# Optimization experiments

Hardware: AMD Instinct MI355X
Metric: run time of the kernel (lower is better)

Reference implementation:

```python
import jax, jax.numpy as jnp
import numpy as np

SEQ, D_IN, D_OUT = 8192, 1024, 1024


def setup_inputs() -> dict:
    key = jax.random.key(0)
    kx, kq, kk, kv = jax.random.split(key, 4)
    # torch nn.Linear weights have shape (out_features, in_features)
    s = 1.0 / np.sqrt(D_IN)
    return {
        "x": jax.random.normal(kx, (SEQ, D_IN), dtype=jnp.float32),
        "Wq": jax.random.uniform(kq, (D_OUT, D_IN), dtype=jnp.float32, minval=-s, maxval=s),
        "Wk": jax.random.uniform(kk, (D_OUT, D_IN), dtype=jnp.float32, minval=-s, maxval=s),
        "Wv": jax.random.uniform(kv, (D_OUT, D_IN), dtype=jnp.float32, minval=-s, maxval=s),
    }


def reference(x, Wq, Wk, Wv):
    # Linear (no bias): y = x @ W.T
    q = x @ Wq.T          # [S, D_OUT]
    k = x @ Wk.T          # [S, D_OUT]
    v = x @ Wv.T          # [S, D_OUT]
    scale = 1.0 / jnp.sqrt(jnp.asarray(k.shape[-1], dtype=x.dtype))
    scores = (q @ k.T) * scale            # [S, S]
    weights = jax.nn.softmax(scores, axis=-1)
    return weights @ v                    # [S, D_OUT]
```

## Files before the change

### kernel.cpp

```cpp
#include <hip/hip_runtime.h>
#include <hip/hip_bf16.h>
#include <stdint.h>


#define SEQ 8192
#define DMODEL 1024
#define LOG2E 1.44269504088896340736f
#define GROUP_M 8

typedef __bf16 bf16_t;
typedef __bf16 bf16x8 __attribute__((ext_vector_type(8)));
typedef float f32x4 __attribute__((ext_vector_type(4)));

__global__ __launch_bounds__(256)
void convert_f32_bf16(const float* __restrict__ in, bf16_t* __restrict__ out, long n) {
    long i = ((long)blockIdx.x * 256 + threadIdx.x) * 4;
    if (i + 3 < n) {
        const float4 v = *(const float4*)(in + i);
        union { ushort4 u; bf16_t b[4]; } p;
        p.b[0] = (bf16_t)v.x; p.b[1] = (bf16_t)v.y;
        p.b[2] = (bf16_t)v.z; p.b[3] = (bf16_t)v.w;
        *(ushort4*)(out + i) = p.u;
    }
}

__global__ __launch_bounds__(256)
void add_f32(float* __restrict__ out, const float* __restrict__ part, long n) {
    long i = ((long)blockIdx.x * 256 + threadIdx.x) * 4;
    if (i + 3 < n) {
        float4 a = *(const float4*)(out + i);
        const float4 b = *(const float4*)(part + i);
        a.x += b.x; a.y += b.y; a.z += b.z; a.w += b.w;
        *(float4*)(out + i) = a;
    }
}

__global__ __launch_bounds__(256)
void zero_f32(float* __restrict__ p, int n) {
    int i = blockIdx.x * 256 + threadIdx.x;
    if (i < n) p[i] = 0.0f;
}

template <typename OutT, int MODE>
__global__ __launch_bounds__(256, 3)
void gemm_nt(const bf16_t* __restrict__ A, const bf16_t* __restrict__ B,
             OutT* __restrict__ C0, OutT* __restrict__ C1,
             float* __restrict__ lsum,
             int M, int N, int Kps, int lda, int ldb, int ldc,
             long plane, int cshift, float alpha)
{
    __shared__ bf16_t As[128 * 64];
    __shared__ bf16_t Bs[128 * 64];

    const int tid  = threadIdx.x;
    const int wave = tid >> 6;
    const int lane = tid & 63;

    const int nbm = M >> 7, nbn = N >> 7;
    const int tiles = nbm * nbn;
    int bid = blockIdx.x;
    const int sid = bid / tiles;
    bid -= sid * tiles;
    const long kbase = (long)sid * Kps;
    OutT* __restrict__ C = sid ? C1 : C0;

    const int per_group = GROUP_M * nbn;
    const int gid   = bid / per_group;
    const int rem   = bid - gid * per_group;
    const int first = gid * GROUP_M;
    const int gsz   = min(nbm - first, GROUP_M);
    const int bm    = first + rem % gsz;
    const int bn    = rem / gsz;
    const long row0 = (long)bm * 128;
    const long col0 = (long)bn * 128;

    const int wm = (wave >> 1) * 64;
    const int wn = (wave & 1) * 64;
    const int lr = lane & 15;
    const int lq = lane >> 4;

    f32x4 acc[4][4] = {};

    for (int k0 = 0; k0 < Kps; k0 += 64) {
        #pragma unroll
        for (int i = 0; i < 4; ++i) {
            const int c = i * 256 + wave * 64 + lane;
            const int r = c >> 3, p = c & 7;
            const int l = (p + r) & 7;
            const bf16_t* ga = A + (row0 + r) * (long)lda + kbase + k0 + l * 8;
            const bf16_t* gb = B + (col0 + r) * (long)ldb + kbase + k0 + l * 8;
            __builtin_amdgcn_global_load_lds(
                (const __attribute__((address_space(1))) uint32_t*)ga,
                (__attribute__((address_space(3))) uint32_t*)(As + (long)c * 8),
                16, 0, 0);
            __builtin_amdgcn_global_load_lds(
                (const __attribute__((address_space(1))) uint32_t*)gb,
                (__attribute__((address_space(3))) uint32_t*)(Bs + (long)c * 8),
                16, 0, 0);
        }
        __syncthreads();

        #pragma unroll
        for (int t = 0; t < 2; ++t) {
            bf16x8 af[4], bfr[4];
            #pragma unroll
            for (int mi = 0; mi < 4; ++mi) {
                const int r = wm + mi * 16 + lr;
                const int p = (t * 4 + lq - r) & 7;
                af[mi] = *(const bf16x8*)(As + (long)r * 64 + p * 8);
            }
            #pragma unroll
            for (int ni = 0; ni < 4; ++ni) {
                const int r = wn + ni * 16 + lr;
                const int p = (t * 4 + lq - r) & 7;
                bfr[ni] = *(const bf16x8*)(Bs + (long)r * 64 + p * 8);
            }
            #pragma unroll
            for (int mi = 0; mi < 4; ++mi)
                #pragma unroll
                for (int ni = 0; ni < 4; ++ni)
                    acc[mi][ni] = __builtin_amdgcn_mfma_f32_16x16x32_bf16(
                        af[mi], bfr[ni], acc[mi][ni], 0, 0, 0);
        }
        __syncthreads();
    }

    OutT* __restrict__ Cb = C + (col0 >> cshift) * plane;
    const int ccol0 = (int)(col0 & (((long)1 << cshift) - 1));

    if (MODE == 1) {
        #pragma unroll
        for (int mi = 0; mi < 4; ++mi)
            #pragma unroll
            for (int rg = 0; rg < 4; ++rg) {
                const long r = row0 + wm + mi * 16 + lq * 4 + rg;
                float part = 0.f;
                #pragma unroll
                for (int ni = 0; ni < 4; ++ni) {
                    const int c = ccol0 + wn + ni * 16 + lr;
                    const float e = exp2f(alpha * acc[mi][ni][rg]);
                    part += e;
                    Cb[r * (long)ldc + c] = (OutT)e;
                }
                part += __shfl_xor(part, 1);
                part += __shfl_xor(part, 2);
                part += __shfl_xor(part, 4);
                part += __shfl_xor(part, 8);
                if (lr == 0) atomicAdd(&lsum[r], part);
            }
    } else if (MODE == 2) {
        #pragma unroll
        for (int mi = 0; mi < 4; ++mi)
            #pragma unroll
            for (int rg = 0; rg < 4; ++rg) {
                const long r = row0 + wm + mi * 16 + lq * 4 + rg;
                const float inv = 1.0f / lsum[r];
                #pragma unroll
                for (int ni = 0; ni < 4; ++ni) {
                    const int c = ccol0 + wn + ni * 16 + lr;
                    Cb[r * (long)ldc + c] = (OutT)(acc[mi][ni][rg] * inv);
                }
            }
    } else {
        #pragma unroll
        for (int mi = 0; mi < 4; ++mi)
            #pragma unroll
            for (int ni = 0; ni < 4; ++ni)
                #pragma unroll
                for (int rg = 0; rg < 4; ++rg) {
                    const long r = row0 + wm + mi * 16 + lq * 4 + rg;
                    const int  c = ccol0 + wn + ni * 16 + lr;
                    Cb[r * (long)ldc + c] = (OutT)(alpha * acc[mi][ni][rg]);
                }
    }
}

__global__ __launch_bounds__(256)
void transpose_bf16(const bf16_t* __restrict__ in, bf16_t* __restrict__ out,
                    int R, int ldin, int ldout)
{
    __shared__ bf16_t tile[32][33];
    const int tx = threadIdx.x & 31;
    const int ty = threadIdx.x >> 5;
    const int c0 = blockIdx.x * 32;
    const int r0 = blockIdx.y * 32;
    #pragma unroll
    for (int j = 0; j < 32; j += 8)
        tile[ty + j][tx] = in[(long)(r0 + ty + j) * ldin + c0 + tx];
    __syncthreads();
    #pragma unroll
    for (int j = 0; j < 32; j += 8)
        out[(long)(c0 + ty + j) * ldout + r0 + tx] = tile[tx][ty + j];
}

extern "C" void kernel_launch(void* const* d_in, const int* in_sizes, int n_in,
                              void* d_out, int out_size, void* d_ws, size_t ws_size,
                              hipStream_t stream)
{
    const float* x  = (const float*)d_in[0];
    const float* Wq = (const float*)d_in[1];
    const float* Wk = (const float*)d_in[2];
    const float* Wv = (const float*)d_in[3];
    float* out = (float*)d_out;

    char* ws = (char*)d_ws;
    const long XN = (long)SEQ * DMODEL;
    const long WN = (long)DMODEL * DMODEL;
    const long SN = (long)SEQ * SEQ;

    bf16_t* xb   = (bf16_t*)ws;
    bf16_t* wcat = (bf16_t*)(ws + XN * 2);
    bf16_t* qb   = (bf16_t*)(ws + XN * 2 + WN * 6);
    bf16_t* kb   = qb + XN;
    bf16_t* vb   = qb + 2 * XN;
    bf16_t* Sb   = (bf16_t*)(ws + XN * 2 + WN * 6 + XN * 6);
    float*  pvp  = (float*)(ws + XN * 2 + WN * 6 + XN * 6 + SN * 2);
    float*  lsum = (float*)(ws + XN * 2 + WN * 6 + XN * 6 + SN * 2 + XN * 4);
    bf16_t* vtb  = xb;

    const size_t base_need = (size_t)(XN * 2 + WN * 6 + XN * 6 + SN * 2);
    const bool use_split = ws_size >= base_need + XN * 4 + SEQ * 4;
    if (!use_split) lsum = (float*)(ws + base_need);

    convert_f32_bf16<<<(int)(XN / 4 / 256), 256, 0, stream>>>(x,  xb, XN);
    convert_f32_bf16<<<(int)(WN / 4 / 256), 256, 0, stream>>>(Wq, wcat,          WN);
    convert_f32_bf16<<<(int)(WN / 4 / 256), 256, 0, stream>>>(Wk, wcat + WN,     WN);
    convert_f32_bf16<<<(int)(WN / 4 / 256), 256, 0, stream>>>(Wv, wcat + 2 * WN, WN);
    zero_f32<<<SEQ / 256, 256, 0, stream>>>(lsum, SEQ);

    dim3 blk(256);
    gemm_nt<bf16_t, 0><<<(SEQ / 128) * (3 * DMODEL / 128), blk, 0, stream>>>(
        xb, wcat, qb, qb, nullptr, SEQ, 3 * DMODEL, DMODEL,
        DMODEL, DMODEL, DMODEL, XN, 10, 1.0f);

    transpose_bf16<<<dim3(DMODEL / 32, SEQ / 32), blk, 0, stream>>>(
        vb, vtb, SEQ, DMODEL, SEQ);

    gemm_nt<bf16_t, 1><<<(SEQ / 128) * (SEQ / 128), blk, 0, stream>>>(
        qb, kb, Sb, Sb, lsum, SEQ, SEQ, DMODEL,
        DMODEL, DMODEL, SEQ, 0, 30, 0.03125f * LOG2E);

    if (use_split) {
        gemm_nt<float, 2><<<2 * (SEQ / 128) * (DMODEL / 128), blk, 0, stream>>>(
            Sb, vtb, out, pvp, lsum, SEQ, DMODEL, SEQ / 2,
            SEQ, SEQ, DMODEL, 0, 30, 1.0f);
        add_f32<<<(int)(XN / 4 / 256), 256, 0, stream>>>(out, pvp, XN);
    } else {
        gemm_nt<float, 2><<<(SEQ / 128) * (DMODEL / 128), blk, 0, stream>>>(
            Sb, vtb, out, out, lsum, SEQ, DMODEL, SEQ,
            SEQ, SEQ, DMODEL, 0, 30, 1.0f);
    }
}
```

Measured before the change: 495.8 us.

## Enlarge GEMM tiles to 256x256 with double-buffered LDS prefetch pipeline

Switches the shared NT GEMM from 128x128 tiles with 256 threads to 256x256 tiles with 512 threads, each wave computing a 128x64 sub-tile. It adds a two-stage LDS double buffer so the global-to-LDS loads for step k+2 are issued between MFMA groups, and uses explicit vmcnt/lgkmcnt waits plus s_setprio. The aim is to hide global load latency and cut the number of times each operand is reloaded. The cost is 128KB of LDS per block, which limits occupancy to one block per CU. Grids also shrink, so the PV and QKV GEMMs launch only about 256 and 384 blocks.

```diff
diff --git a/kernel.cpp b/kernel.cpp
--- a/kernel.cpp
+++ b/kernel.cpp
@@ -42,21 +42,21 @@
 }
 
 template <typename OutT, int MODE>
-__global__ __launch_bounds__(256, 3)
+__global__ __launch_bounds__(512, 2)
 void gemm_nt(const bf16_t* __restrict__ A, const bf16_t* __restrict__ B,
              OutT* __restrict__ C0, OutT* __restrict__ C1,
              float* __restrict__ lsum,
              int M, int N, int Kps, int lda, int ldb, int ldc,
              long plane, int cshift, float alpha)
 {
-    __shared__ bf16_t As[128 * 64];
-    __shared__ bf16_t Bs[128 * 64];
+    __shared__ bf16_t As[2][256 * 64];
+    __shared__ bf16_t Bs[2][256 * 64];
 
     const int tid  = threadIdx.x;
     const int wave = tid >> 6;
     const int lane = tid & 63;
 
-    const int nbm = M >> 7, nbn = N >> 7;
+    const int nbm = M >> 8, nbn = N >> 8;
     const int tiles = nbm * nbn;
     int bid = blockIdx.x;
     const int sid = bid / tiles;
@@ -71,66 +71,129 @@
     const int gsz   = min(nbm - first, GROUP_M);
     const int bm    = first + rem % gsz;
     const int bn    = rem / gsz;
-    const long row0 = (long)bm * 128;
-    const long col0 = (long)bn * 128;
-
-    const int wm = (wave >> 1) * 64;
-    const int wn = (wave & 1) * 64;
+    const long row0 = (long)bm * 256;
+    const long col0 = (long)bn * 256;
+
+    const int wm = (wave >> 2) * 128;
+    const int wn = (wave & 3) * 64;
     const int lr = lane & 15;
     const int lq = lane >> 4;
 
-    f32x4 acc[4][4] = {};
-
-    for (int k0 = 0; k0 < Kps; k0 += 64) {
-        #pragma unroll
-        for (int i = 0; i < 4; ++i) {
-            const int c = i * 256 + wave * 64 + lane;
-            const int r = c >> 3, p = c & 7;
-            const int l = (p + r) & 7;
-            const bf16_t* ga = A + (row0 + r) * (long)lda + kbase + k0 + l * 8;
-            const bf16_t* gb = B + (col0 + r) * (long)ldb + kbase + k0 + l * 8;
-            __builtin_amdgcn_global_load_lds(
-                (const __attribute__((address_space(1))) uint32_t*)ga,
-                (__attribute__((address_space(3))) uint32_t*)(As + (long)c * 8),
-                16, 0, 0);
-            __builtin_amdgcn_global_load_lds(
-                (const __attribute__((address_space(1))) uint32_t*)gb,
-                (__attribute__((address_space(3))) uint32_t*)(Bs + (long)c * 8),
-                16, 0, 0);
-        }
-        __syncthreads();
-
-        #pragma unroll
-        for (int t = 0; t < 2; ++t) {
-            bf16x8 af[4], bfr[4];
-            #pragma unroll
-            for (int mi = 0; mi < 4; ++mi) {
-                const int r = wm + mi * 16 + lr;
-                const int p = (t * 4 + lq - r) & 7;
-                af[mi] = *(const bf16x8*)(As + (long)r * 64 + p * 8);
-            }
-            #pragma unroll
-            for (int ni = 0; ni < 4; ++ni) {
-                const int r = wn + ni * 16 + lr;
-                const int p = (t * 4 + lq - r) & 7;
-                bfr[ni] = *(const bf16x8*)(Bs + (long)r * 64 + p * 8);
-            }
-            #pragma unroll
-            for (int mi = 0; mi < 4; ++mi)
-                #pragma unroll
-                for (int ni = 0; ni < 4; ++ni)
-                    acc[mi][ni] = __builtin_amdgcn_mfma_f32_16x16x32_bf16(
-                        af[mi], bfr[ni], acc[mi][ni], 0, 0, 0);
-        }
-        __syncthreads();
-    }
+    const int rt = tid >> 3;
+    const int sl = ((tid & 7) + rt) & 7;
+    const bf16_t* pa = A + (row0 + rt) * (long)lda + kbase + sl * 8;
+    const bf16_t* pb = B + (col0 + rt) * (long)ldb + kbase + sl * 8;
+
+    const int p0  = (lq - lr) & 7;
+    const int p1  = p0 ^ 4;
+    const int oA0 = (wm + lr) * 64 + p0 * 8;
+    const int oA1 = (wm + lr) * 64 + p1 * 8;
+    const int oB0 = (wn + lr) * 64 + p0 * 8;
+    const int oB1 = (wn + lr) * 64 + p1 * 8;
+
+    const int nt = Kps >> 6;
+
+    f32x4 acc[8][4] = {};
+
+#define STAGE2(kt, bsel, i0)                                                    \
+    {                                                                           \
+        _Pragma("unroll")                                                       \
+        for (int ii = 0; ii < 2; ++ii) {                                        \
+            const int i = (i0) + ii;                                            \
+            const bf16_t* ga = pa + (long)(kt) * 64 + (long)i * 64 * lda;       \
+            const bf16_t* gb = pb + (long)(kt) * 64 + (long)i * 64 * ldb;       \
+            __builtin_amdgcn_global_load_lds(                                   \
+                (const __attribute__((address_space(1))) uint32_t*)ga,          \
+                (__attribute__((address_space(3))) uint32_t*)(As[bsel] + i * 4096 + tid * 8), \
+                16, 0, 0);                                                      \
+            __builtin_amdgcn_global_load_lds(                                   \
+                (const __attribute__((address_space(1))) uint32_t*)gb,          \
+                (__attribute__((address_space(3))) uint32_t*)(Bs[bsel] + i * 4096 + tid * 8), \
+                16, 0, 0);                                                      \
+        }                                                                       \
+    }
+
+    STAGE2(0, 0, 0); STAGE2(0, 0, 2);
+    if (nt > 1) { STAGE2(1, 1, 0); STAGE2(1, 1, 2); }
+
+    int cur = 0;
+    for (int t = 0; t < nt; ++t) {
+        const bf16_t* as = As[cur];
+        const bf16_t* bs = Bs[cur];
+
+        if (t + 1 < nt) { asm volatile("s_waitcnt vmcnt(8)" ::: "memory"); }
+        else            { asm volatile("s_waitcnt vmcnt(0)" ::: "memory"); }
+        __builtin_amdgcn_s_barrier();
+
+        bf16x8 a0[8], b0[4], a1[8], b1[4];
+        #pragma unroll
+        for (int mi = 0; mi < 8; ++mi)
+            a0[mi] = *(const bf16x8*)(as + oA0 + mi * 1024);
+        #pragma unroll
+        for (int ni = 0; ni < 4; ++ni)
+            b0[ni] = *(const bf16x8*)(bs + oB0 + ni * 1024);
+
+        __builtin_amdgcn_s_setprio(1);
+        #pragma unroll
+        for (int mi = 0; mi < 4; ++mi)
+            #pragma unroll
+            for (int ni = 0; ni < 4; ++ni)
+                acc[mi][ni] = __builtin_amdgcn_mfma_f32_16x16x32_bf16(
+                    a0[mi], b0[ni], acc[mi][ni], 0, 0, 0);
+        __builtin_amdgcn_s_setprio(0);
+
+        #pragma unroll
+        for (int mi = 0; mi < 8; ++mi)
+            a1[mi] = *(const bf16x8*)(as + oA1 + mi * 1024);
+        #pragma unroll
+        for (int ni = 0; ni < 4; ++ni)
+            b1[ni] = *(const bf16x8*)(bs + oB1 + ni * 1024);
+
+        __builtin_amdgcn_s_setprio(1);
+        #pragma unroll
+        for (int mi = 4; mi < 8; ++mi)
+            #pragma unroll
+            for (int ni = 0; ni < 4; ++ni)
+                acc[mi][ni] = __builtin_amdgcn_mfma_f32_16x16x32_bf16(
+                    a0[mi], b0[ni], acc[mi][ni], 0, 0, 0);
+        __builtin_amdgcn_s_setprio(0);
+
+        asm volatile("s_waitcnt lgkmcnt(0)" ::: "memory");
+        __builtin_amdgcn_sched_barrier(0);
+        __builtin_amdgcn_s_barrier();
+
+        if (t + 2 < nt) STAGE2(t + 2, cur, 0);
+
+        __builtin_amdgcn_s_setprio(1);
+        #pragma unroll
+        for (int mi = 0; mi < 4; ++mi)
+            #pragma unroll
+            for (int ni = 0; ni < 4; ++ni)
+                acc[mi][ni] = __builtin_amdgcn_mfma_f32_16x16x32_bf16(
+                    a1[mi], b1[ni], acc[mi][ni], 0, 0, 0);
+        __builtin_amdgcn_s_setprio(0);
+
+        if (t + 2 < nt) STAGE2(t + 2, cur, 2);
+
+        __builtin_amdgcn_s_setprio(1);
+        #pragma unroll
+        for (int mi = 4; mi < 8; ++mi)
+            #pragma unroll
+            for (int ni = 0; ni < 4; ++ni)
+                acc[mi][ni] = __builtin_amdgcn_mfma_f32_16x16x32_bf16(
+                    a1[mi], b1[ni], acc[mi][ni], 0, 0, 0);
+        __builtin_amdgcn_s_setprio(0);
+
+        cur ^= 1;
+    }
+#undef STAGE2
 
     OutT* __restrict__ Cb = C + (col0 >> cshift) * plane;
     const int ccol0 = (int)(col0 & (((long)1 << cshift) - 1));
 
     if (MODE == 1) {
         #pragma unroll
-        for (int mi = 0; mi < 4; ++mi)
+        for (int mi = 0; mi < 8; ++mi)
             #pragma unroll
             for (int rg = 0; rg < 4; ++rg) {
                 const long r = row0 + wm + mi * 16 + lq * 4 + rg;
@@ -150,7 +213,7 @@
             }
     } else if (MODE == 2) {
         #pragma unroll
-        for (int mi = 0; mi < 4; ++mi)
+        for (int mi = 0; mi < 8; ++mi)
             #pragma unroll
             for (int rg = 0; rg < 4; ++rg) {
                 const long r = row0 + wm + mi * 16 + lq * 4 + rg;
@@ -163,7 +226,7 @@
             }
     } else {
         #pragma unroll
-        for (int mi = 0; mi < 4; ++mi)
+        for (int mi = 0; mi < 8; ++mi)
             #pragma unroll
             for (int ni = 0; ni < 4; ++ni)
                 #pragma unroll
@@ -228,25 +291,26 @@
     convert_f32_bf16<<<(int)(WN / 4 / 256), 256, 0, stream>>>(Wv, wcat + 2 * WN, WN);
     zero_f32<<<SEQ / 256, 256, 0, stream>>>(lsum, SEQ);
 
-    dim3 blk(256);
-    gemm_nt<bf16_t, 0><<<(SEQ / 128) * (3 * DMODEL / 128), blk, 0, stream>>>(
+    dim3 blk256(256);
+    dim3 blk512(512);
+    gemm_nt<bf16_t, 0><<<(SEQ / 256) * (3 * DMODEL / 256), blk512, 0, stream>>>(
         xb, wcat, qb, qb, nullptr, SEQ, 3 * DMODEL, DMODEL,
         DMODEL, DMODEL, DMODEL, XN, 10, 1.0f);
 
-    transpose_bf16<<<dim3(DMODEL / 32, SEQ / 32), blk, 0, stream>>>(
+    transpose_bf16<<<dim3(DMODEL / 32, SEQ / 32), blk256, 0, stream>>>(
         vb, vtb, SEQ, DMODEL, SEQ);
 
-    gemm_nt<bf16_t, 1><<<(SEQ / 128) * (SEQ / 128), blk, 0, stream>>>(
+    gemm_nt<bf16_t, 1><<<(SEQ / 256) * (SEQ / 256), blk512, 0, stream>>>(
         qb, kb, Sb, Sb, lsum, SEQ, SEQ, DMODEL,
         DMODEL, DMODEL, SEQ, 0, 30, 0.03125f * LOG2E);
 
     if (use_split) {
-        gemm_nt<float, 2><<<2 * (SEQ / 128) * (DMODEL / 128), blk, 0, stream>>>(
+        gemm_nt<float, 2><<<2 * (SEQ / 256) * (DMODEL / 256), blk512, 0, stream>>>(
             Sb, vtb, out, pvp, lsum, SEQ, DMODEL, SEQ / 2,
             SEQ, SEQ, DMODEL, 0, 30, 1.0f);
         add_f32<<<(int)(XN / 4 / 256), 256, 0, stream>>>(out, pvp, XN);
     } else {
-        gemm_nt<float, 2><<<(SEQ / 128) * (DMODEL / 128), blk, 0, stream>>>(
+        gemm_nt<float, 2><<<(SEQ / 256) * (DMODEL / 256), blk512, 0, stream>>>(
             Sb, vtb, out, out, lsum, SEQ, DMODEL, SEQ,
             SEQ, SEQ, DMODEL, 0, 30, 1.0f);
     }
```

After: 474.9 us. 1.04x faster.

## Halve GEMM K-tile to 32, precompute swizzled addresses, remap blocks across XCDs

Applied to the files above, without the earlier changes.

Shrinks the K step of the bf16 GEMM from 64 to 32. That halves LDS per block and lets the load and fragment addresses be computed once with a new 4-way swizzle. It also remaps block IDs so consecutive tiles are spread across 8 chiplets (XCDs) for better L2 locality. The smaller K tile means twice as many barrier pairs per unit of work, with less MFMA work between them to hide load latency. It may raise occupancy, but sync overhead could dominate.

```diff
diff --git a/kernel.cpp b/kernel.cpp
--- a/kernel.cpp
+++ b/kernel.cpp
@@ -49,8 +49,8 @@
              int M, int N, int Kps, int lda, int ldb, int ldc,
              long plane, int cshift, float alpha)
 {
-    __shared__ bf16_t As[128 * 64];
-    __shared__ bf16_t Bs[128 * 64];
+    __shared__ bf16_t As[128 * 32];
+    __shared__ bf16_t Bs[128 * 32];
 
     const int tid  = threadIdx.x;
     const int wave = tid >> 6;
@@ -63,6 +63,9 @@
     bid -= sid * tiles;
     const long kbase = (long)sid * Kps;
     OutT* __restrict__ C = sid ? C1 : C0;
+
+    const int cpx = tiles >> 3;
+    bid = (bid & 7) * cpx + (bid >> 3);
 
     const int per_group = GROUP_M * nbn;
     const int gid   = bid / per_group;
@@ -79,49 +82,46 @@
     const int lr = lane & 15;
     const int lq = lane >> 4;
 
+    const int rt = tid >> 2;
+    const int sl = ((tid & 3) + ((tid >> 4) & 3)) & 3;
+    const bf16_t* pa = A + (row0 + rt) * (long)lda + kbase + sl * 8;
+    const bf16_t* pb = B + (col0 + rt) * (long)ldb + kbase + sl * 8;
+
+    const int p0  = (lq - ((lr >> 2) & 3)) & 3;
+    const int oA  = (wm + lr) * 32 + p0 * 8;
+    const int oB  = (wn + lr) * 32 + p0 * 8;
+
     f32x4 acc[4][4] = {};
 
-    for (int k0 = 0; k0 < Kps; k0 += 64) {
-        #pragma unroll
-        for (int i = 0; i < 4; ++i) {
-            const int c = i * 256 + wave * 64 + lane;
-            const int r = c >> 3, p = c & 7;
-            const int l = (p + r) & 7;
-            const bf16_t* ga = A + (row0 + r) * (long)lda + kbase + k0 + l * 8;
-            const bf16_t* gb = B + (col0 + r) * (long)ldb + kbase + k0 + l * 8;
+    for (int k0 = 0; k0 < Kps; k0 += 32) {
+        #pragma unroll
+        for (int i = 0; i < 2; ++i) {
+            const bf16_t* ga = pa + k0 + (long)i * 64 * lda;
+            const bf16_t* gb = pb + k0 + (long)i * 64 * ldb;
             __builtin_amdgcn_global_load_lds(
                 (const __attribute__((address_space(1))) uint32_t*)ga,
-                (__attribute__((address_space(3))) uint32_t*)(As + (long)c * 8),
+                (__attribute__((address_space(3))) uint32_t*)(As + (long)(i * 256 + tid) * 8),
                 16, 0, 0);
             __builtin_amdgcn_global_load_lds(
                 (const __attribute__((address_space(1))) uint32_t*)gb,
-                (__attribute__((address_space(3))) uint32_t*)(Bs + (long)c * 8),
+                (__attribute__((address_space(3))) uint32_t*)(Bs + (long)(i * 256 + tid) * 8),
                 16, 0, 0);
         }
         __syncthreads();
 
-        #pragma unroll
-        for (int t = 0; t < 2; ++t) {
-            bf16x8 af[4], bfr[4];
-            #pragma unroll
-            for (int mi = 0; mi < 4; ++mi) {
-                const int r = wm + mi * 16 + lr;
-                const int p = (t * 4 + lq - r) & 7;
-                af[mi] = *(const bf16x8*)(As + (long)r * 64 + p * 8);
-            }
-            #pragma unroll
-            for (int ni = 0; ni < 4; ++ni) {
-                const int r = wn + ni * 16 + lr;
-                const int p = (t * 4 + lq - r) & 7;
-                bfr[ni] = *(const bf16x8*)(Bs + (long)r * 64 + p * 8);
-            }
-            #pragma unroll
-            for (int mi = 0; mi < 4; ++mi)
-                #pragma unroll
-                for (int ni = 0; ni < 4; ++ni)
-                    acc[mi][ni] = __builtin_amdgcn_mfma_f32_16x16x32_bf16(
-                        af[mi], bfr[ni], acc[mi][ni], 0, 0, 0);
-        }
+        bf16x8 af[4], bfr[4];
+        #pragma unroll
+        for (int mi = 0; mi < 4; ++mi)
+            af[mi] = *(const bf16x8*)(As + oA + mi * 512);
+        #pragma unroll
+        for (int ni = 0; ni < 4; ++ni)
+            bfr[ni] = *(const bf16x8*)(Bs + oB + ni * 512);
+        #pragma unroll
+        for (int mi = 0; mi < 4; ++mi)
+            #pragma unroll
+            for (int ni = 0; ni < 4; ++ni)
+                acc[mi][ni] = __builtin_amdgcn_mfma_f32_16x16x32_bf16(
+                    af[mi], bfr[ni], acc[mi][ni], 0, 0, 0);
         __syncthreads();
     }
 
```

New measurement: 503.0 us. About the same (+1.4%).
